# Optimization experiments

Measured on AMD Instinct MI355X. Metric: run time of the kernel, lower is better.

Reference implementation:

```python
import jax, jax.numpy as jnp
import numpy as np

B, N, D = 8, 1024, 512
H, HD = 8, 64          # heads, head_dim
E_EDGES = 4096         # num edges (!= N -> mean-pool branch)
NE, NSH, TOPK = 8, 2, 2  # routed experts, shared experts, top-k
DH = 2 * D             # expert hidden dim
EPS = 1e-5
HALT_BONUS = 0.1
AUX_ALPHA = 0.01


def _ln(x, g, b):
    mu = jnp.mean(x, -1, keepdims=True)
    var = jnp.mean(jnp.square(x - mu), -1, keepdims=True)
    return (x - mu) * jax.lax.rsqrt(var + EPS) * g + b


def setup_inputs() -> dict:
    key = jax.random.key(0)
    ks = jax.random.split(key, 20)
    w = lambda k, shp: jax.random.normal(k, shp, jnp.float32) * 0.02
    return {
        'h': jax.random.normal(ks[0], (B, N, D), jnp.float32),
        'edge_features': jax.random.normal(ks[1], (B, E_EDGES, D), jnp.float32),
        'log_A': jnp.zeros((D,), jnp.float32),
        'B_w': w(ks[2], (D, D)), 'B_b': jnp.zeros((D,), jnp.float32),
        'Wq': w(ks[3], (D, D)), 'bq': jnp.zeros((D,), jnp.float32),
        'Wk': w(ks[4], (D, D)), 'bk': jnp.zeros((D,), jnp.float32),
        'Wv': w(ks[5], (D, D)), 'bv': jnp.zeros((D,), jnp.float32),
        'Wo': w(ks[6], (D, D)), 'bo': jnp.zeros((D,), jnp.float32),
        'n1_g': jnp.ones((D,), jnp.float32), 'n1_b': jnp.zeros((D,), jnp.float32),
        'n2_g': jnp.ones((D,), jnp.float32), 'n2_b': jnp.zeros((D,), jnp.float32),
        'n3_g': jnp.ones((D,), jnp.float32), 'n3_b': jnp.zeros((D,), jnp.float32),
        'gate_w': w(ks[7], (D, NE)), 'gate_b': jnp.zeros((NE,), jnp.float32),
        'eW1': w(ks[8], (NE, D, DH)), 'eb1': jnp.zeros((NE, DH), jnp.float32),
        'eW2': w(ks[9], (NE, DH, D)), 'eb2': jnp.zeros((NE, D), jnp.float32),
        'sW1': w(ks[10], (NSH, D, DH)), 'sb1': jnp.zeros((NSH, DH), jnp.float32),
        'sW2': w(ks[11], (NSH, DH, D)), 'sb2': jnp.zeros((NSH, D), jnp.float32),
        'hW1': w(ks[12], (D, D // 2)), 'hb1': jnp.zeros((D // 2,), jnp.float32),
        'hW2': w(ks[13], (D // 2, 1)), 'hb2': jnp.zeros((1,), jnp.float32),
    }


def reference(h, edge_features, log_A, B_w, B_b, Wq, bq, Wk, bk, Wv, bv, Wo, bo,
              n1_g, n1_b, n2_g, n2_b, n3_g, n3_b, gate_w, gate_b,
              eW1, eb1, eW2, eb2, sW1, sb1, sW2, sb2, hW1, hb1, hW2, hb2):
    # --- LTI: h_decay + mean-pooled edge injection (num_edges != num_nodes) ---
    A = -jnp.exp(log_A)                                   # spectral constraint
    edge_inj = edge_features @ B_w + B_b                  # [B,E,D]
    edge_inj = jnp.mean(edge_inj, axis=1, keepdims=True)  # [B,1,D] broadcast
    h_lti = _ln(A * h + edge_inj, n1_g, n1_b)

    # --- attention (faithful to source: no head/node transpose -> [B,N,H,H] scores) ---
    q = (h_lti @ Wq + bq).reshape(B, N, H, HD)
    k = (h_lti @ Wk + bk).reshape(B, N, H, HD)
    v = (h_lti @ Wv + bv).reshape(B, N, H, HD)
    scores = jnp.einsum('bnhd,bngd->bnhg', q, k) / jnp.sqrt(jnp.float32(HD))
    attn = jax.nn.softmax(scores, axis=-1)                # dropout = identity (eval)
    h_attn = jnp.einsum('bnhg,bngd->bnhd', attn, v).reshape(B, N, D) @ Wo + bo
    h2 = _ln(h_lti + h_attn, n2_g, n2_b)

    # --- SparseMoE: top-k routed + shared experts, load-balance aux loss ---
    x = h2.reshape(-1, D)                                 # [T,D]
    T = x.shape[0]
    probs = jax.nn.softmax(x @ gate_w + gate_b, axis=-1)  # [T,NE]
    topv, topi = jax.lax.top_k(probs, TOPK)
    topv = topv / jnp.sum(topv, -1, keepdims=True)        # renormalize top-k
    w_full = jnp.sum(jax.nn.one_hot(topi, NE, dtype=x.dtype) * topv[..., None], axis=1)  # [T,NE]
    hid = jax.nn.silu(jnp.einsum('td,edh->teh', x, eW1) + eb1)   # [T,NE,DH]
    eout = jnp.einsum('teh,ehd->ted', hid, eW2) + eb2            # [T,NE,D]
    routed = jnp.einsum('te,ted->td', w_full, eout)
    shid = jax.nn.silu(jnp.einsum('td,sdh->tsh', x, sW1) + sb1)
    shared = jnp.sum(jnp.einsum('tsh,shd->tsd', shid, sW2) + sb2, axis=1)
    h_moe = (routed + shared).reshape(B, N, D)
    frac = jnp.mean(jnp.sum(jax.nn.one_hot(topi, NE, dtype=x.dtype), axis=1), axis=0)  # tokens per expert
    pmean = jnp.mean(probs, axis=0)
    moe_loss = AUX_ALPHA * NE * jnp.sum(frac * pmean)

    h3 = _ln(h2 + h_moe, n3_g, n3_b)                      # dropout = identity (eval)

    # --- stability loss (source uses .item() -> detached constant) ---
    stab = jax.lax.stop_gradient(jnp.maximum(jnp.max(jnp.exp(log_A)) - 0.95, 0.0))

    # --- ACT halting (cumsum_halt=None path) ---
    halt_logits = (jnp.tanh(h3 @ hW1 + hb1) @ hW2 + hb2)[..., 0]  # [B,N]
    halt_prob = jax.nn.sigmoid(halt_logits)
    cumsum_halt = halt_prob                                # zeros + prob * active(=1)
    return h3, cumsum_halt, halt_prob, stab + moe_loss
```

## Files before the change

kernel.cpp:

```cpp
#include <hip/hip_runtime.h>
#include <hip/hip_bf16.h>

#define TT 8192
#define DD 512

typedef unsigned short u16;
typedef __attribute__((ext_vector_type(8))) short short8;
typedef __attribute__((ext_vector_type(4))) float f32x4;

__device__ __forceinline__ u16 f2b(float f) {
  union { float f; unsigned int i; } w; w.f = f;
  unsigned int x = w.i;
  unsigned int r = (x + 0x7FFFu + ((x >> 16) & 1u)) >> 16;
  if ((x & 0x7F800000u) == 0x7F800000u) r = x >> 16;
  return (u16)r;
}
__device__ __forceinline__ float b2f(u16 u) {
  union { unsigned int i; float f; } w; w.i = ((unsigned int)u) << 16; return w.f;
}

__device__ __forceinline__ void blockReduce2(float& a, float& b, float* s4a, float* s4b) {
  #pragma unroll
  for (int off = 32; off; off >>= 1) { a += __shfl_xor(a, off); b += __shfl_xor(b, off); }
  int wid = threadIdx.x >> 6;
  if ((threadIdx.x & 63) == 0) { s4a[wid] = a; s4b[wid] = b; }
  __syncthreads();
  a = s4a[0] + s4a[1] + s4a[2] + s4a[3];
  b = s4b[0] + s4b[1] + s4b[2] + s4b[3];
}

__global__ __launch_bounds__(256) void k_zero(float* __restrict__ esum) {
  esum[blockIdx.x * 256 + threadIdx.x] = 0.f;
}

__global__ __launch_bounds__(256) void k_zero4(float4* __restrict__ p) {
  p[(size_t)blockIdx.x * 256 + threadIdx.x] = make_float4(0.f, 0.f, 0.f, 0.f);
}

__global__ __launch_bounds__(256) void k_esum(const float* __restrict__ ef, float* __restrict__ esum) {
  int b = blockIdx.x, ec = blockIdx.y, tid = threadIdx.x;
  float a0 = 0.f, a1 = 0.f;
  const float* base = ef + ((size_t)b * 4096 + (size_t)ec * 128) * 512;
  for (int e = 0; e < 128; ++e) {
    a0 += base[(size_t)e * 512 + tid];
    a1 += base[(size_t)e * 512 + tid + 256];
  }
  atomicAdd(&esum[b * 512 + tid], a0);
  atomicAdd(&esum[b * 512 + tid + 256], a1);
}

__global__ __launch_bounds__(256) void k_einj(const float* __restrict__ esum,
                                              const float* __restrict__ Bw, const float* __restrict__ Bb,
                                              float* __restrict__ einj) {
  int idx = blockIdx.x * 256 + threadIdx.x;
  int b = idx >> 9, dp = idx & 511;
  float a = Bb[dp];
  const float inv = 1.f / 4096.f;
  for (int d = 0; d < 512; ++d)
    a = fmaf(esum[b * 512 + d] * inv, Bw[d * 512 + dp], a);
  einj[idx] = a;
}

__global__ __launch_bounds__(256) void k_wsplit(const float* __restrict__ Wq, const float* __restrict__ Wk,
                                                const float* __restrict__ Wv, const float* __restrict__ Wo,
                                                u16* __restrict__ outh, u16* __restrict__ outl) {
  __shared__ float st[64][65];
  int z = blockIdx.z;
  const float* W = z == 0 ? Wq : (z == 1 ? Wk : (z == 2 ? Wv : Wo));
  int k0 = blockIdx.x << 6, n0 = blockIdx.y << 6;
  int tid = threadIdx.x;
  int r = tid >> 2, c4 = (tid & 3) << 4;
  #pragma unroll
  for (int j = 0; j < 16; j += 4) {
    float4 v = *(const float4*)(W + (size_t)(k0 + r) * 512 + n0 + c4 + j);
    st[c4 + j + 0][r] = v.x; st[c4 + j + 1][r] = v.y;
    st[c4 + j + 2][r] = v.z; st[c4 + j + 3][r] = v.w;
  }
  __syncthreads();
  int n = tid >> 2, kb = (tid & 3) << 4;
  u16 h8[8] __attribute__((aligned(16)));
  u16 l8[8] __attribute__((aligned(16)));
  size_t obase = (size_t)z * 262144 + (size_t)(n0 + n) * 512 + k0 + kb;
  #pragma unroll
  for (int half = 0; half < 2; ++half) {
    #pragma unroll
    for (int j = 0; j < 8; ++j) {
      float val = st[n][kb + half * 8 + j];
      h8[j] = f2b(val);
      l8[j] = f2b(val - b2f(h8[j]));
    }
    *(uint4*)(outh + obase + half * 8) = *(uint4*)h8;
    *(uint4*)(outl + obase + half * 8) = *(uint4*)l8;
  }
}

__global__ __launch_bounds__(256) void k_wt(const float* __restrict__ W, u16* __restrict__ Wt,
                                            int K, int N) {
  __shared__ float st[64][65];
  int z = blockIdx.z;
  W += (size_t)z * K * N; Wt += (size_t)z * K * N;
  int k0 = blockIdx.x << 6, n0 = blockIdx.y << 6;
  int tid = threadIdx.x;
  int r = tid >> 2, c4 = (tid & 3) << 4;
  #pragma unroll
  for (int j = 0; j < 16; j += 4) {
    float4 v = *(const float4*)(W + (size_t)(k0 + r) * N + n0 + c4 + j);
    st[c4 + j + 0][r] = v.x; st[c4 + j + 1][r] = v.y;
    st[c4 + j + 2][r] = v.z; st[c4 + j + 3][r] = v.w;
  }
  __syncthreads();
  int n = tid >> 2, kb = (tid & 3) << 4;
  u16 h8[8] __attribute__((aligned(16)));
  size_t obase = (size_t)(n0 + n) * K + k0 + kb;
  #pragma unroll
  for (int half = 0; half < 2; ++half) {
    #pragma unroll
    for (int j = 0; j < 8; ++j) h8[j] = f2b(st[n][kb + half * 8 + j]);
    *(uint4*)(Wt + obase + half * 8) = *(uint4*)h8;
  }
}

__global__ __launch_bounds__(256) void k_lti(const float* __restrict__ h, const float* __restrict__ lA,
                                             const float* __restrict__ einj,
                                             const float* __restrict__ g, const float* __restrict__ be,
                                             u16* __restrict__ Xh, u16* __restrict__ Xl, int seg0) {
  __shared__ float sa[4], sb[4];
  int rowg = seg0 + blockIdx.x, b = rowg >> 10, tid = threadIdx.x;
  int d0 = tid, d1 = tid + 256;
  size_t gbase = (size_t)rowg * 512;
  size_t lbase = (size_t)blockIdx.x * 512;
  float v0 = -expf(lA[d0]) * h[gbase + d0] + einj[b * 512 + d0];
  float v1 = -expf(lA[d1]) * h[gbase + d1] + einj[b * 512 + d1];
  float s = v0 + v1, ss = v0 * v0 + v1 * v1;
  blockReduce2(s, ss, sa, sb);
  float mu = s * (1.f / 512.f);
  float var = fmaxf(ss * (1.f / 512.f) - mu * mu, 0.f);
  float r = rsqrtf(var + 1e-5f);
  float o0 = (v0 - mu) * r * g[d0] + be[d0];
  float o1 = (v1 - mu) * r * g[d1] + be[d1];
  u16 h0 = f2b(o0), h1 = f2b(o1);
  Xh[lbase + d0] = h0; Xl[lbase + d0] = f2b(o0 - b2f(h0));
  Xh[lbase + d1] = h1; Xl[lbase + d1] = f2b(o1 - b2f(h1));
}

__global__ __launch_bounds__(256) void k_ln_res2(const u16* __restrict__ Xh, const u16* __restrict__ Xl,
                                                 const float* __restrict__ Bv,
                                                 const float* __restrict__ g, const float* __restrict__ be,
                                                 float* __restrict__ outf, u16* __restrict__ outb) {
  __shared__ float sa[4], sb[4];
  int tid = threadIdx.x, d0 = tid, d1 = tid + 256;
  size_t base = (size_t)blockIdx.x * 512;
  float v0 = b2f(Xh[base + d0]) + b2f(Xl[base + d0]) + Bv[base + d0];
  float v1 = b2f(Xh[base + d1]) + b2f(Xl[base + d1]) + Bv[base + d1];
  float s = v0 + v1, ss = v0 * v0 + v1 * v1;
  blockReduce2(s, ss, sa, sb);
  float mu = s * (1.f / 512.f);
  float var = fmaxf(ss * (1.f / 512.f) - mu * mu, 0.f);
  float r = rsqrtf(var + 1e-5f);
  float o0 = (v0 - mu) * r * g[d0] + be[d0];
  float o1 = (v1 - mu) * r * g[d1] + be[d1];
  outf[base + d0] = o0;
  outf[base + d1] = o1;
  if (outb) { outb[base + d0] = f2b(o0); outb[base + d1] = f2b(o1); }
}

__global__ __launch_bounds__(256) void k_ln_res(const float* __restrict__ A, const float* __restrict__ Bv,
                                                const float* __restrict__ g, const float* __restrict__ be,
                                                float* __restrict__ outf) {
  __shared__ float sa[4], sb[4];
  int tid = threadIdx.x, d0 = tid, d1 = tid + 256;
  size_t base = (size_t)blockIdx.x * 512;
  float v0 = A[base + d0] + Bv[base + d0];
  float v1 = A[base + d1] + Bv[base + d1];
  float s = v0 + v1, ss = v0 * v0 + v1 * v1;
  blockReduce2(s, ss, sa, sb);
  float mu = s * (1.f / 512.f);
  float var = fmaxf(ss * (1.f / 512.f) - mu * mu, 0.f);
  float r = rsqrtf(var + 1e-5f);
  outf[base + d0] = (v0 - mu) * r * g[d0] + be[d0];
  outf[base + d1] = (v1 - mu) * r * g[d1] + be[d1];
}

template<int NOUT>
__global__ __launch_bounds__(256) void gemm_sp2(
    const u16* __restrict__ Xh, const u16* __restrict__ Xl, int lda,
    const u16* __restrict__ Wth, const u16* __restrict__ Wtl,
    const float* __restrict__ b0c, const float* __restrict__ b1c, const float* __restrict__ b2c,
    float* __restrict__ C0, float* __restrict__ C1, float* __restrict__ C2) {
  const float* bias = b0c; float* C = C0;
  const u16* Wh = Wth; const u16* Wl = Wtl;
  if (NOUT == 3) {
    int z = blockIdx.z;
    Wh += (size_t)z * 262144; Wl += (size_t)z * 262144;
    if (z == 1) { bias = b1c; C = C1; }
    else if (z == 2) { bias = b2c; C = C2; }
  }
  const int bm = blockIdx.y << 7, bn = blockIdx.x << 7;
  __shared__ u16 Ah[128][40];
  __shared__ u16 Al[128][40];
  __shared__ u16 Bh[128][40];
  __shared__ u16 Bl[128][40];
  const int tid = threadIdx.x;
  const int sr = tid >> 1, sk = (tid & 1) << 4;
  const int wv = tid >> 6, lane = tid & 63, q = lane >> 4, m16 = lane & 15;
  const int wr = (wv >> 1) << 6, wc = (wv & 1) << 6;
  f32x4 acc[4][4];
  #pragma unroll
  for (int m = 0; m < 4; ++m)
    #pragma unroll
    for (int n = 0; n < 4; ++n)
      #pragma unroll
      for (int i = 0; i < 4; ++i) acc[m][n][i] = 0.f;

  for (int k0 = 0; k0 < 512; k0 += 32) {
    __syncthreads();
    const size_t ao_ = (size_t)(bm + sr) * lda + k0 + sk;
    const size_t bo_ = (size_t)(bn + sr) * 512 + k0 + sk;
    *(uint4*)&Ah[sr][sk]     = *(const uint4*)(Xh + ao_);
    *(uint4*)&Ah[sr][sk + 8] = *(const uint4*)(Xh + ao_ + 8);
    *(uint4*)&Al[sr][sk]     = *(const uint4*)(Xl + ao_);
    *(uint4*)&Al[sr][sk + 8] = *(const uint4*)(Xl + ao_ + 8);
    *(uint4*)&Bh[sr][sk]     = *(const uint4*)(Wh + bo_);
    *(uint4*)&Bh[sr][sk + 8] = *(const uint4*)(Wh + bo_ + 8);
    *(uint4*)&Bl[sr][sk]     = *(const uint4*)(Wl + bo_);
    *(uint4*)&Bl[sr][sk + 8] = *(const uint4*)(Wl + bo_ + 8);
    __syncthreads();
    short8 ah[4], al[4];
    #pragma unroll
    for (int m = 0; m < 4; ++m) {
      ah[m] = *(const short8*)&Ah[wr + m * 16 + m16][q * 8];
      al[m] = *(const short8*)&Al[wr + m * 16 + m16][q * 8];
    }
    #pragma unroll
    for (int n = 0; n < 4; ++n) {
      short8 bh = *(const short8*)&Bh[wc + n * 16 + m16][q * 8];
      short8 bl = *(const short8*)&Bl[wc + n * 16 + m16][q * 8];
      #pragma unroll
      for (int m = 0; m < 4; ++m) {
        acc[m][n] = __builtin_amdgcn_mfma_f32_16x16x32_bf16(ah[m], bh, acc[m][n], 0, 0, 0);
        acc[m][n] = __builtin_amdgcn_mfma_f32_16x16x32_bf16(al[m], bh, acc[m][n], 0, 0, 0);
        acc[m][n] = __builtin_amdgcn_mfma_f32_16x16x32_bf16(ah[m], bl, acc[m][n], 0, 0, 0);
      }
    }
  }
  #pragma unroll
  for (int n = 0; n < 4; ++n) {
    int col = bn + wc + n * 16 + m16;
    float bb = bias[col];
    #pragma unroll
    for (int m = 0; m < 4; ++m) {
      #pragma unroll
      for (int i = 0; i < 4; ++i) {
        int rl = bm + wr + m * 16 + q * 4 + i;
        C[(size_t)rl * 512 + col] = acc[m][n][i] + bb;
      }
    }
  }
}

__global__ __launch_bounds__(64) void k_attn(const float* __restrict__ q, const float* __restrict__ k,
                                             const float* __restrict__ v,
                                             u16* __restrict__ aohl) {
  __shared__ float qs[512], ks[512], vs[512], at[64];
  size_t t = blockIdx.x;
  int lane = threadIdx.x;
  for (int i = lane; i < 512; i += 64) {
    qs[i] = q[t * 512 + i]; ks[i] = k[t * 512 + i]; vs[i] = v[t * 512 + i];
  }
  __syncthreads();
  int h = lane >> 3, g = lane & 7;
  float s = 0.f;
  #pragma unroll 8
  for (int d = 0; d < 64; ++d) s = fmaf(qs[h * 64 + d], ks[g * 64 + d], s);
  s *= 0.125f;
  float m = s;
  #pragma unroll
  for (int off = 1; off < 8; off <<= 1) m = fmaxf(m, __shfl_xor(m, off));
  float ex = expf(s - m);
  float sum = ex;
  #pragma unroll
  for (int off = 1; off < 8; off <<= 1) sum += __shfl_xor(sum, off);
  at[lane] = ex / sum;
  __syncthreads();
  #pragma unroll
  for (int j = 0; j < 8; ++j) {
    int d = lane + j * 64, hh = d >> 6, hd = d & 63;
    float acc = 0.f;
    #pragma unroll
    for (int gg = 0; gg < 8; ++gg) acc = fmaf(at[hh * 8 + gg], vs[gg * 64 + hd], acc);
    u16 hi = f2b(acc);
    aohl[t * 1024 + d] = hi;
    aohl[t * 1024 + 512 + d] = f2b(acc - b2f(hi));
  }
}

__global__ __launch_bounds__(256) void k_gateA(const float* __restrict__ h2, const float* __restrict__ gw,
                                               const float* __restrict__ gb, float* __restrict__ probs,
                                               int* __restrict__ sel, float2* __restrict__ wpair) {
  int lane = threadIdx.x & 63, wid = threadIdx.x >> 6;
  int t = blockIdx.x * 4 + wid;
  const float* x = h2 + (size_t)t * 512;
  float acc[8] = {};
  for (int d = lane; d < 512; d += 64) {
    float xv = x[d];
    float4 g0 = *(const float4*)(gw + d * 8);
    float4 g1 = *(const float4*)(gw + d * 8 + 4);
    acc[0] = fmaf(xv, g0.x, acc[0]); acc[1] = fmaf(xv, g0.y, acc[1]);
    acc[2] = fmaf(xv, g0.z, acc[2]); acc[3] = fmaf(xv, g0.w, acc[3]);
    acc[4] = fmaf(xv, g1.x, acc[4]); acc[5] = fmaf(xv, g1.y, acc[5]);
    acc[6] = fmaf(xv, g1.z, acc[6]); acc[7] = fmaf(xv, g1.w, acc[7]);
  }
  #pragma unroll
  for (int off = 32; off; off >>= 1)
    #pragma unroll
    for (int e = 0; e < 8; ++e) acc[e] += __shfl_xor(acc[e], off);
  if (lane == 0) {
    float m = -1e30f;
    #pragma unroll
    for (int e = 0; e < 8; ++e) { acc[e] += gb[e]; m = fmaxf(m, acc[e]); }
    float p[8], sum = 0.f;
    #pragma unroll
    for (int e = 0; e < 8; ++e) { p[e] = expf(acc[e] - m); sum += p[e]; }
    float inv = 1.f / sum;
    #pragma unroll
    for (int e = 0; e < 8; ++e) { p[e] *= inv; probs[t * 8 + e] = p[e]; }
    int i1 = 0; float m1 = p[0];
    #pragma unroll
    for (int e = 1; e < 8; ++e) if (p[e] > m1) { m1 = p[e]; i1 = e; }
    int i2 = -1; float m2 = -1.f;
    #pragma unroll
    for (int e = 0; e < 8; ++e) if (e != i1 && p[e] > m2) { m2 = p[e]; i2 = e; }
    if (i2 < 0) i2 = (i1 + 1) & 7;
    float den = m1 + m2;
    float invs = (den > 0.f) ? 1.f / den : 0.f;
    sel[t] = i1 | (i2 << 4);
    wpair[t] = make_float2(m1 * invs, m2 * invs);
  }
}

__global__ __launch_bounds__(256) void k_gateB(const int* __restrict__ sel, const float2* __restrict__ wpair,
                                               int* __restrict__ toklist, float* __restrict__ wlist,
                                               int* __restrict__ cnt) {
  int e = blockIdx.x;
  int tid = threadIdx.x, lane = tid & 63, wv = tid >> 6;
  __shared__ int wsum[4];
  int base = 0;
  for (int t0 = 0; t0 < 8192; t0 += 256) {
    int t = t0 + tid;
    int s = sel[t];
    int i1 = s & 15, i2 = (s >> 4) & 15;
    bool f = (i1 == e) || (i2 == e);
    float wt = (i1 == e) ? wpair[t].x : ((i2 == e) ? wpair[t].y : 0.f);
    unsigned long long m = __ballot(f);
    int rank = __popcll(m & ((1ull << lane) - 1ull));
    int wtot = __popcll(m);
    if (lane == 0) wsum[wv] = wtot;
    __syncthreads();
    int prev = 0;
    for (int ww = 0; ww < wv; ++ww) prev += wsum[ww];
    int tot = wsum[0] + wsum[1] + wsum[2] + wsum[3];
    if (f) {
      int pos = base + prev + rank;
      toklist[e * 8192 + pos] = t;
      wlist[e * 8192 + pos] = wt;
    }
    base += tot;
    __syncthreads();
  }
  if (tid == 0) cnt[e] = base;
}

template<int XMODE, int ACT, int OUTMODE, int EXPERT>
__global__ __launch_bounds__(256) void mfma_gemm(
    const float* __restrict__ Xf, const u16* __restrict__ Xb,
    const float* __restrict__ Wg, const float* __restrict__ biasg,
    float* __restrict__ C, u16* __restrict__ C16,
    const int* __restrict__ toklist, const float* __restrict__ wlist,
    const int* __restrict__ cnt, int M, int K, int N, int chunk0,
    size_t hidstride, float* __restrict__ moe) {
  int e = EXPERT ? blockIdx.z : 0;
  const float* W = Wg + (size_t)e * K * N;
  const float* bias = biasg + (size_t)e * N;
  int Mloc = M;
  if (EXPERT) {
    int ce = cnt[e]; if (ce > 8192) ce = 8192;
    Mloc = ce - chunk0;
    if (XMODE == 1) Xb += (size_t)e * hidstride;
    if (OUTMODE == 2) C16 += (size_t)e * hidstride;
  }
  const int bm = blockIdx.y << 6, bn = blockIdx.x << 6;
  if (EXPERT && bm >= Mloc) return;
  __shared__ u16 As[64][40];
  __shared__ u16 Bs[64][40];
  __shared__ int rows[64];
  const int tid = threadIdx.x;
  if (EXPERT && XMODE == 2 && tid < 64) {
    int ce = cnt[e]; if (ce > 8192) ce = 8192;
    int r = chunk0 + bm + tid;
    rows[tid] = toklist[e * 8192 + (r < ce ? r : chunk0)] & 8191;
  }
  const int srow = tid >> 2;
  const int skg = (tid & 3) << 3;
  const int wv = tid >> 6, lane = tid & 63, q = lane >> 4, m16 = lane & 15;
  f32x4 acc[4];
  #pragma unroll
  for (int c = 0; c < 4; ++c)
    #pragma unroll
    for (int i = 0; i < 4; ++i) acc[c][i] = 0.f;

  for (int k0 = 0; k0 < K; k0 += 32) {
    __syncthreads();
    {
      u16 a8[8] __attribute__((aligned(16)));
      if (XMODE == 1) {
        *(uint4*)a8 = *(const uint4*)(Xb + (size_t)(bm + srow) * K + k0 + skg);
      } else {
        const float* src = (XMODE == 2) ? (Xf + (size_t)rows[srow] * K + k0 + skg)
                                        : (Xf + (size_t)(bm + srow) * K + k0 + skg);
        float4 x0 = *(const float4*)(src);
        float4 x1 = *(const float4*)(src + 4);
        a8[0] = f2b(x0.x); a8[1] = f2b(x0.y); a8[2] = f2b(x0.z); a8[3] = f2b(x0.w);
        a8[4] = f2b(x1.x); a8[5] = f2b(x1.y); a8[6] = f2b(x1.z); a8[7] = f2b(x1.w);
      }
      *(uint4*)&As[srow][skg] = *(uint4*)a8;
    }
    {
      u16 b8[8] __attribute__((aligned(16)));
      const float* src = W + (size_t)(k0 + skg) * N + bn + srow;
      #pragma unroll
      for (int j = 0; j < 8; ++j) b8[j] = f2b(src[(size_t)j * N]);
      *(uint4*)&Bs[srow][skg] = *(uint4*)b8;
    }
    __syncthreads();
    short8 af = *(const short8*)&As[wv * 16 + m16][q * 8];
    #pragma unroll
    for (int c = 0; c < 4; ++c) {
      short8 bf = *(const short8*)&Bs[c * 16 + m16][q * 8];
      acc[c] = __builtin_amdgcn_mfma_f32_16x16x32_bf16(af, bf, acc[c], 0, 0, 0);
    }
  }
  #pragma unroll
  for (int c = 0; c < 4; ++c) {
    int col = bn + c * 16 + m16;
    float bb = bias[col];
    #pragma unroll
    for (int i = 0; i < 4; ++i) {
      int rl = bm + wv * 16 + q * 4 + i;
      if (EXPERT && rl >= Mloc) continue;
      float v = acc[c][i] + bb;
      if (ACT == 1) v = v / (1.f + expf(-v));
      else if (ACT == 2) v = tanhf(v);
      if (OUTMODE == 0) C[(size_t)rl * N + col] = v;
      else if (OUTMODE == 1) C[(size_t)rl * N + col] += v;
      else if (OUTMODE == 2) C16[(size_t)rl * N + col] = f2b(v);
      else {
        int rg = chunk0 + rl;
        int tok = toklist[e * 8192 + rg] & 8191;
        float wt = wlist[e * 8192 + rg];
        atomicAdd(&moe[(size_t)tok * 512 + col], v * wt);
      }
    }
  }
}

template<int XMODE, int ACT, int OUTMODE, int EXPERT>
__global__ __launch_bounds__(512, 4) void mfma_gemm3(
    const u16* __restrict__ Xb, const u16* __restrict__ Wt, const float* __restrict__ biasg,
    float* __restrict__ C, u16* __restrict__ C16,
    const int* __restrict__ toklist, const float* __restrict__ wlist,
    const int* __restrict__ cnt, int M, int K, int N, int chunk0,
    size_t hidstride, float* __restrict__ moe) {
  int e = EXPERT ? blockIdx.z : 0;
  const u16* W = Wt + (size_t)e * K * N;
  const float* bias = biasg + (size_t)e * N;
  int Mloc = M;
  if (EXPERT == 1) {
    int ce = cnt[e]; if (ce > 8192) ce = 8192;
    Mloc = ce - chunk0;
  }
  if (EXPERT) {
    if (XMODE == 3) Xb += (size_t)e * hidstride;
    if (OUTMODE == 2) C16 += (size_t)e * hidstride;
  }
  const int bm = blockIdx.y << 7, bn = blockIdx.x << 7;
  if (EXPERT == 1 && bm >= Mloc) return;
  __shared__ u16 As[2][128][40];
  __shared__ u16 Bs[2][128][40];
  __shared__ int rows[128];
  const int tid = threadIdx.x;
  if (EXPERT == 1 && XMODE == 2) {
    if (tid < 128) {
      int ce = cnt[e]; if (ce > 8192) ce = 8192;
      int r = chunk0 + bm + tid;
      rows[tid] = toklist[e * 8192 + (r < ce ? r : chunk0)] & 8191;
    }
    __syncthreads();
  }
  const int sr = tid >> 2, sk = (tid & 3) << 3;
  const int wv = tid >> 6, lane = tid & 63, q = lane >> 4, m16 = lane & 15;
  const int wr = (wv >> 2) << 6;
  const int wc = (wv & 3) << 5;
  const u16* arow = (XMODE == 2) ? (Xb + (size_t)rows[sr] * K) : (Xb + (size_t)(bm + sr) * K);
  const u16* brow = W + (size_t)(bn + sr) * K;
  f32x4 acc[4][2];
  #pragma unroll
  for (int m = 0; m < 4; ++m)
    #pragma unroll
    for (int n = 0; n < 2; ++n)
      #pragma unroll
      for (int i = 0; i < 4; ++i) acc[m][n][i] = 0.f;

  uint4 ar = *(const uint4*)(arow + sk);
  uint4 br = *(const uint4*)(brow + sk);
  *(uint4*)&As[0][sr][sk] = ar;
  *(uint4*)&Bs[0][sr][sk] = br;
  __syncthreads();
  int cur = 0;
  for (int k0 = 0; k0 < K; k0 += 32) {
    if (k0 + 32 < K) {
      ar = *(const uint4*)(arow + k0 + 32 + sk);
      br = *(const uint4*)(brow + k0 + 32 + sk);
    }
    short8 af[4];
    #pragma unroll
    for (int m = 0; m < 4; ++m)
      af[m] = *(const short8*)&As[cur][wr + m * 16 + m16][q * 8];
    short8 bf[2];
    #pragma unroll
    for (int n = 0; n < 2; ++n)
      bf[n] = *(const short8*)&Bs[cur][wc + n * 16 + m16][q * 8];
    #pragma unroll
    for (int n = 0; n < 2; ++n)
      #pragma unroll
      for (int m = 0; m < 4; ++m)
        acc[m][n] = __builtin_amdgcn_mfma_f32_16x16x32_bf16(af[m], bf[n], acc[m][n], 0, 0, 0);
    if (k0 + 32 < K) {
      *(uint4*)&As[cur ^ 1][sr][sk] = ar;
      *(uint4*)&Bs[cur ^ 1][sr][sk] = br;
      __syncthreads();
      cur ^= 1;
    }
  }
  #pragma unroll
  for (int n = 0; n < 2; ++n) {
    int col = bn + wc + n * 16 + m16;
    float bb = bias[col];
    #pragma unroll
    for (int m = 0; m < 4; ++m) {
      #pragma unroll
      for (int i = 0; i < 4; ++i) {
        int rl = bm + wr + m * 16 + q * 4 + i;
        if (EXPERT == 1 && rl >= Mloc) continue;
        float v = acc[m][n][i] + bb;
        if (ACT == 1) v = v / (1.f + expf(-v));
        if (OUTMODE == 0) C[(size_t)rl * N + col] = v;
        else if (OUTMODE == 1) C[(size_t)rl * N + col] += v;
        else if (OUTMODE == 2) C16[(size_t)rl * N + col] = f2b(v);
        else if (OUTMODE == 3) {
          int rg = chunk0 + rl;
          int tok = toklist[e * 8192 + rg] & 8191;
          float wt = wlist[e * 8192 + rg];
          atomicAdd(&moe[(size_t)tok * 512 + col], v * wt);
        } else {
          atomicAdd(&C[(size_t)rl * N + col], v);
        }
      }
    }
  }
}

__global__ __launch_bounds__(256) void k_halt(const u16* __restrict__ hh, const float* __restrict__ hW2,
                                              const float* __restrict__ hb2, float* __restrict__ out) {
  int lane = threadIdx.x & 63, wid = threadIdx.x >> 6;
  int t = blockIdx.x * 4 + wid;
  const u16* x = hh + (size_t)t * 256;
  float a = b2f(x[lane]) * hW2[lane] + b2f(x[lane + 64]) * hW2[lane + 64] +
            b2f(x[lane + 128]) * hW2[lane + 128] + b2f(x[lane + 192]) * hW2[lane + 192];
  #pragma unroll
  for (int off = 32; off; off >>= 1) a += __shfl_xor(a, off);
  if (lane == 0) {
    float p = 1.f / (1.f + expf(-(a + hb2[0])));
    out[4194304 + t] = p;
    out[4194304 + 8192 + t] = p;
  }
}

__global__ __launch_bounds__(256) void k_final(const float* __restrict__ probs, const int* __restrict__ cnt,
                                               const float* __restrict__ lA, float* __restrict__ out) {
  __shared__ float sp[4][8];
  __shared__ float sm[4];
  int tid = threadIdx.x, lane = tid & 63, wid = tid >> 6;
  float part[8] = {};
  for (int i = tid; i < 8192; i += 256) {
    const float* p = probs + i * 8;
    #pragma unroll
    for (int e = 0; e < 8; ++e) part[e] += p[e];
  }
  #pragma unroll
  for (int off = 32; off; off >>= 1)
    #pragma unroll
    for (int e = 0; e < 8; ++e) part[e] += __shfl_xor(part[e], off);
  float mx = 0.f;
  for (int d = tid; d < 512; d += 256) mx = fmaxf(mx, expf(lA[d]));
  #pragma unroll
  for (int off = 32; off; off >>= 1) mx = fmaxf(mx, __shfl_xor(mx, off));
  if (lane == 0) {
    #pragma unroll
    for (int e = 0; e < 8; ++e) sp[wid][e] = part[e];
    sm[wid] = mx;
  }
  __syncthreads();
  if (tid == 0) {
    float loss = 0.f;
    for (int e = 0; e < 8; ++e) {
      float pm = (sp[0][e] + sp[1][e] + sp[2][e] + sp[3][e]) * (1.f / 8192.f);
      int c = cnt[e]; if (c > 8192) c = 8192;
      loss += (float)c * (1.f / 8192.f) * pm;
    }
    loss *= 0.01f * 8.f;
    float mall = fmaxf(fmaxf(sm[0], sm[1]), fmaxf(sm[2], sm[3]));
    out[4194304 + 16384] = fmaxf(mall - 0.95f, 0.f) + loss;
  }
}

extern "C" void kernel_launch(void* const* d_in, const int* in_sizes, int n_in,
                              void* d_out, int out_size, void* d_ws, size_t ws_size,
                              hipStream_t stream) {
  const float* h   = (const float*)d_in[0];
  const float* ef  = (const float*)d_in[1];
  const float* lA  = (const float*)d_in[2];
  const float* Bw  = (const float*)d_in[3];
  const float* Bb  = (const float*)d_in[4];
  const float* Wq  = (const float*)d_in[5];  const float* bq  = (const float*)d_in[6];
  const float* Wk  = (const float*)d_in[7];  const float* bk  = (const float*)d_in[8];
  const float* Wv  = (const float*)d_in[9];  const float* bv  = (const float*)d_in[10];
  const float* Wo  = (const float*)d_in[11]; const float* bo  = (const float*)d_in[12];
  const float* n1g = (const float*)d_in[13]; const float* n1b = (const float*)d_in[14];
  const float* n2g = (const float*)d_in[15]; const float* n2b = (const float*)d_in[16];
  const float* n3g = (const float*)d_in[17]; const float* n3b = (const float*)d_in[18];
  const float* gw  = (const float*)d_in[19]; const float* gb  = (const float*)d_in[20];
  const float* eW1 = (const float*)d_in[21]; const float* eb1 = (const float*)d_in[22];
  const float* eW2 = (const float*)d_in[23]; const float* eb2 = (const float*)d_in[24];
  const float* sW1 = (const float*)d_in[25]; const float* sb1 = (const float*)d_in[26];
  const float* sW2 = (const float*)d_in[27]; const float* sb2 = (const float*)d_in[28];
  const float* hW1 = (const float*)d_in[29]; const float* hb1 = (const float*)d_in[30];
  const float* hW2 = (const float*)d_in[31]; const float* hb2 = (const float*)d_in[32];
  float* out = (float*)d_out;
  float* ws = (float*)d_ws;

  const size_t R = (size_t)TT * DD;
  const size_t SM = 155648 + 73744;
  size_t wsf = ws_size / 4;
  int S; size_t ARENA;
  bool FAST;
  if (wsf >= 6 * R + SM)      { S = 8192; ARENA = 4 * R; FAST = true; }
  else if (wsf >= 3 * R + SM) { S = 2048; ARENA = R; FAST = false; }
  else                        { S = 512;  ARENA = 1048576; FAST = false; }
  const int CAPE = (int)(ARENA / 4096);
  const int NCH  = 8192 / CAPE;
  const size_t HIDSTRIDE = (size_t)CAPE * 1024;
  const int CAPS = (ARENA / 512 >= 8192) ? 8192 : (int)(ARENA / 512);

  float* f_h2  = ws;
  float* f_moe = ws + R;
  float* arena = ws + 2 * R;
  const size_t SD = (size_t)S * 512;
  u16* f_xh = (u16*)arena;
  u16* f_xl = f_xh + SD;
  float* f_q = arena + SD;
  float* f_k = arena + 2 * SD;
  float* f_v = arena + 3 * SD;
  u16* f_aohl = (u16*)f_q;
  float* f_hp = f_k;
  u16* f_wh = (u16*)f_moe;
  u16* f_wl = f_wh + 4 * 262144;
  u16* f_hid = (u16*)arena;
  u16* f_hh  = (u16*)arena;
  u16* a16 = (u16*)arena;
  const int CAPE_F = 2048, NCH_F = 4;
  const size_t HSF = (size_t)CAPE_F * 1024;
  u16* f_hidF = a16;
  u16* f_eW1t = a16 + 16777216;
  u16* f_eW2t = a16 + 20971520;
  u16* f_h2b  = a16 + 25165824;
  u16* f_sW1t = a16 + 29360128;
  u16* f_sW2t = a16 + 30408704;
  float* smr = ws + 2 * R + ARENA;
  float* f_esum = smr;
  float* f_einj = smr + 4096;
  float* f_probs = smr + 8192;
  float2* f_wpair = (float2*)(smr + 8192 + 65536);
  float* f_wlist = smr + 8192 + 65536 + 16384;
  int* ip = (int*)(smr + 8192 + 65536 + 16384 + 65536);
  int* sel = ip; int* cnt = ip + 8192; int* toklist = ip + 8192 + 16;

  k_zero<<<16, 256, 0, stream>>>(f_esum);
  k_esum<<<dim3(8, 32), 256, 0, stream>>>(ef, f_esum);
  k_einj<<<16, 256, 0, stream>>>(f_esum, Bw, Bb, f_einj);
  k_wsplit<<<dim3(8, 8, 4), 256, 0, stream>>>(Wq, Wk, Wv, Wo, f_wh, f_wl);

  for (int s = 0; s < TT / S; ++s) {
    int seg0 = s * S;
    k_lti<<<S, 256, 0, stream>>>(h, lA, f_einj, n1g, n1b, f_xh, f_xl, seg0);
    gemm_sp2<3><<<dim3(4, S / 128, 3), 256, 0, stream>>>(
        f_xh, f_xl, 512, f_wh, f_wl, bq, bk, bv, f_q, f_k, f_v);
    k_attn<<<S, 64, 0, stream>>>(f_q, f_k, f_v, f_aohl);
    gemm_sp2<1><<<dim3(4, S / 128, 1), 256, 0, stream>>>(
        f_aohl, f_aohl + 512, 1024, f_wh + 3 * 262144, f_wl + 3 * 262144,
        bo, nullptr, nullptr, f_hp, nullptr, nullptr);
    k_ln_res2<<<S, 256, 0, stream>>>(f_xh, f_xl, f_hp, n2g, n2b,
                                     f_h2 + (size_t)seg0 * 512,
                                     FAST ? f_h2b + (size_t)seg0 * 512 : nullptr);
  }

  k_gateA<<<TT / 4, 256, 0, stream>>>(f_h2, gw, gb, f_probs, sel, f_wpair);
  k_gateB<<<8, 256, 0, stream>>>(sel, f_wpair, toklist, f_wlist, cnt);

  if (FAST) {
    k_zero4<<<4096, 256, 0, stream>>>((float4*)f_moe);
    k_wt<<<dim3(8, 16, 8), 256, 0, stream>>>(eW1, f_eW1t, 512, 1024);
    k_wt<<<dim3(16, 8, 8), 256, 0, stream>>>(eW2, f_eW2t, 1024, 512);
    k_wt<<<dim3(8, 16, 2), 256, 0, stream>>>(sW1, f_sW1t, 512, 1024);
    k_wt<<<dim3(16, 8, 2), 256, 0, stream>>>(sW2, f_sW2t, 1024, 512);

    mfma_gemm3<1,1,2,2><<<dim3(8, 64, 2), 512, 0, stream>>>(
        f_h2b, f_sW1t, sb1, nullptr, f_hidF, nullptr, nullptr, nullptr,
        TT, 512, 1024, 0, (size_t)TT * 1024, nullptr);
    mfma_gemm3<3,0,4,2><<<dim3(4, 64, 2), 512, 0, stream>>>(
        f_hidF, f_sW2t, sb2, f_moe, nullptr, nullptr, nullptr, nullptr,
        TT, 1024, 512, 0, (size_t)TT * 1024, nullptr);

    for (int c = 0; c < NCH_F; ++c) {
      mfma_gemm3<2,1,2,1><<<dim3(8, CAPE_F / 128, 8), 512, 0, stream>>>(
          f_h2b, f_eW1t, eb1, nullptr, f_hidF, toklist, nullptr, cnt,
          CAPE_F, 512, 1024, c * CAPE_F, HSF, nullptr);
      mfma_gemm3<3,0,3,1><<<dim3(4, CAPE_F / 128, 8), 512, 0, stream>>>(
          f_hidF, f_eW2t, eb2, nullptr, nullptr, toklist, f_wlist, cnt,
          CAPE_F, 1024, 512, c * CAPE_F, HSF, f_moe);
    }
  } else {
    for (int sx = 0; sx < 2; ++sx)
      for (int c = 0; c < TT / CAPS; ++c) {
        const float* xs = f_h2 + (size_t)c * CAPS * 512;
        float* ms = f_moe + (size_t)c * CAPS * 512;
        mfma_gemm<0,1,2,0><<<dim3(16, CAPS / 64), 256, 0, stream>>>(
            xs, nullptr, sW1 + (size_t)sx * 524288, sb1 + sx * 1024,
            nullptr, f_hid, nullptr, nullptr, nullptr, CAPS, 512, 1024, 0, 0, nullptr);
        if (sx == 0)
          mfma_gemm<1,0,0,0><<<dim3(8, CAPS / 64), 256, 0, stream>>>(
              nullptr, f_hid, sW2, sb2, ms, nullptr, nullptr, nullptr, nullptr, CAPS, 1024, 512, 0, 0, nullptr);
        else
          mfma_gemm<1,0,1,0><<<dim3(8, CAPS / 64), 256, 0, stream>>>(
              nullptr, f_hid, sW2 + 524288, sb2 + 512, ms, nullptr, nullptr, nullptr, nullptr, CAPS, 1024, 512, 0, 0, nullptr);
      }
    for (int c = 0; c < NCH; ++c) {
      mfma_gemm<2,1,2,1><<<dim3(16, CAPE / 64, 8), 256, 0, stream>>>(
          f_h2, nullptr, eW1, eb1, nullptr, f_hid, toklist, nullptr, cnt,
          CAPE, 512, 1024, c * CAPE, HIDSTRIDE, nullptr);
      mfma_gemm<1,0,3,1><<<dim3(8, CAPE / 64, 8), 256, 0, stream>>>(
          nullptr, f_hid, eW2, eb2, nullptr, nullptr, toklist, f_wlist, cnt,
          CAPE, 1024, 512, c * CAPE, HIDSTRIDE, f_moe);
    }
  }

  k_ln_res<<<TT, 256, 0, stream>>>(f_h2, f_moe, n3g, n3b, out);
  mfma_gemm<0,2,2,0><<<dim3(4, 128), 256, 0, stream>>>(
      out, nullptr, hW1, hb1, nullptr, f_hh, nullptr, nullptr, nullptr, TT, 512, 256, 0, 0, nullptr);
  k_halt<<<TT / 4, 256, 0, stream>>>(f_hh, hW2, hb2, out);
  k_final<<<1, 256, 0, stream>>>(f_probs, cnt, lA, out);
}
```

Before: 713.7 us.

## Double-buffer split-bf16 attention GEMM and move halting head to bf16 MFMA path

The split-precision attention projection GEMM now uses 512 threads with a 4x2 wave layout and double-buffered shared memory, prefetching the next K-slice into registers while the MFMAs run. This is meant to hide global-load latency and drop one barrier per iteration. In the fast path, the final layernorm also writes a bf16 copy of its output. The halting MLP's first layer then runs through the bf16 mfma_gemm3 kernel with a transposed weight and a new tanh activation in the epilogue. That trades some precision in the halting head and adds a small transpose launch.

```diff
diff --git a/kernel.cpp b/kernel.cpp
--- a/kernel.cpp
+++ b/kernel.cpp
@@ -166,7 +166,7 @@
 
 __global__ __launch_bounds__(256) void k_ln_res(const float* __restrict__ A, const float* __restrict__ Bv,
                                                 const float* __restrict__ g, const float* __restrict__ be,
-                                                float* __restrict__ outf) {
+                                                float* __restrict__ outf, u16* __restrict__ outb) {
   __shared__ float sa[4], sb[4];
   int tid = threadIdx.x, d0 = tid, d1 = tid + 256;
   size_t base = (size_t)blockIdx.x * 512;
@@ -177,12 +177,15 @@
   float mu = s * (1.f / 512.f);
   float var = fmaxf(ss * (1.f / 512.f) - mu * mu, 0.f);
   float r = rsqrtf(var + 1e-5f);
-  outf[base + d0] = (v0 - mu) * r * g[d0] + be[d0];
-  outf[base + d1] = (v1 - mu) * r * g[d1] + be[d1];
+  float o0 = (v0 - mu) * r * g[d0] + be[d0];
+  float o1 = (v1 - mu) * r * g[d1] + be[d1];
+  outf[base + d0] = o0;
+  outf[base + d1] = o1;
+  if (outb) { outb[base + d0] = f2b(o0); outb[base + d1] = f2b(o1); }
 }
 
 template<int NOUT>
-__global__ __launch_bounds__(256) void gemm_sp2(
+__global__ __launch_bounds__(512, 4) void gemm_sp3(
     const u16* __restrict__ Xh, const u16* __restrict__ Xl, int lda,
     const u16* __restrict__ Wth, const u16* __restrict__ Wtl,
     const float* __restrict__ b0c, const float* __restrict__ b1c, const float* __restrict__ b2c,
@@ -196,55 +199,72 @@
     else if (z == 2) { bias = b2c; C = C2; }
   }
   const int bm = blockIdx.y << 7, bn = blockIdx.x << 7;
-  __shared__ u16 Ah[128][40];
-  __shared__ u16 Al[128][40];
-  __shared__ u16 Bh[128][40];
-  __shared__ u16 Bl[128][40];
+  __shared__ u16 Ah[2][128][40];
+  __shared__ u16 Al[2][128][40];
+  __shared__ u16 Bh[2][128][40];
+  __shared__ u16 Bl[2][128][40];
   const int tid = threadIdx.x;
-  const int sr = tid >> 1, sk = (tid & 1) << 4;
+  const int sr = tid >> 2, sk = (tid & 3) << 3;
   const int wv = tid >> 6, lane = tid & 63, q = lane >> 4, m16 = lane & 15;
-  const int wr = (wv >> 1) << 6, wc = (wv & 1) << 6;
-  f32x4 acc[4][4];
+  const int wr = (wv >> 2) << 6;
+  const int wc = (wv & 3) << 5;
+  const u16* ahr = Xh + (size_t)(bm + sr) * lda;
+  const u16* alr = Xl + (size_t)(bm + sr) * lda;
+  const u16* bhr = Wh + (size_t)(bn + sr) * 512;
+  const u16* blr = Wl + (size_t)(bn + sr) * 512;
+  f32x4 acc[4][2];
   #pragma unroll
   for (int m = 0; m < 4; ++m)
     #pragma unroll
-    for (int n = 0; n < 4; ++n)
+    for (int n = 0; n < 2; ++n)
       #pragma unroll
       for (int i = 0; i < 4; ++i) acc[m][n][i] = 0.f;
 
+  uint4 rah = *(const uint4*)(ahr + sk);
+  uint4 ral = *(const uint4*)(alr + sk);
+  uint4 rbh = *(const uint4*)(bhr + sk);
+  uint4 rbl = *(const uint4*)(blr + sk);
+  *(uint4*)&Ah[0][sr][sk] = rah;
+  *(uint4*)&Al[0][sr][sk] = ral;
+  *(uint4*)&Bh[0][sr][sk] = rbh;
+  *(uint4*)&Bl[0][sr][sk] = rbl;
+  __syncthreads();
+  int cur = 0;
   for (int k0 = 0; k0 < 512; k0 += 32) {
-    __syncthreads();
-    const size_t ao_ = (size_t)(bm + sr) * lda + k0 + sk;
-    const size_t bo_ = (size_t)(bn + sr) * 512 + k0 + sk;
-    *(uint4*)&Ah[sr][sk]     = *(const uint4*)(Xh + ao_);
-    *(uint4*)&Ah[sr][sk + 8] = *(const uint4*)(Xh + ao_ + 8);
-    *(uint4*)&Al[sr][sk]     = *(const uint4*)(Xl + ao_);
-    *(uint4*)&Al[sr][sk + 8] = *(const uint4*)(Xl + ao_ + 8);
-    *(uint4*)&Bh[sr][sk]     = *(const uint4*)(Wh + bo_);
-    *(uint4*)&Bh[sr][sk + 8] = *(const uint4*)(Wh + bo_ + 8);
-    *(uint4*)&Bl[sr][sk]     = *(const uint4*)(Wl + bo_);
-    *(uint4*)&Bl[sr][sk + 8] = *(const uint4*)(Wl + bo_ + 8);
-    __syncthreads();
-    short8 ah[4], al[4];
+    if (k0 + 32 < 512) {
+      rah = *(const uint4*)(ahr + k0 + 32 + sk);
+      ral = *(const uint4*)(alr + k0 + 32 + sk);
+      rbh = *(const uint4*)(bhr + k0 + 32 + sk);
+      rbl = *(const uint4*)(blr + k0 + 32 + sk);
+    }
+    short8 ahf[4], alf[4];
     #pragma unroll
     for (int m = 0; m < 4; ++m) {
-      ah[m] = *(const short8*)&Ah[wr + m * 16 + m16][q * 8];
-      al[m] = *(const short8*)&Al[wr + m * 16 + m16][q * 8];
-    }
-    #pragma unroll
-    for (int n = 0; n < 4; ++n) {
-      short8 bh = *(const short8*)&Bh[wc + n * 16 + m16][q * 8];
-      short8 bl = *(const short8*)&Bl[wc + n * 16 + m16][q * 8];
+      ahf[m] = *(const short8*)&Ah[cur][wr + m * 16 + m16][q * 8];
+      alf[m] = *(const short8*)&Al[cur][wr + m * 16 + m16][q * 8];
+    }
+    #pragma unroll
+    for (int n = 0; n < 2; ++n) {
+      short8 bhf = *(const short8*)&Bh[cur][wc + n * 16 + m16][q * 8];
+      short8 blf = *(const short8*)&Bl[cur][wc + n * 16 + m16][q * 8];
       #pragma unroll
       for (int m = 0; m < 4; ++m) {
-        acc[m][n] = __builtin_amdgcn_mfma_f32_16x16x32_bf16(ah[m], bh, acc[m][n], 0, 0, 0);
-        acc[m][n] = __builtin_amdgcn_mfma_f32_16x16x32_bf16(al[m], bh, acc[m][n], 0, 0, 0);
-        acc[m][n] = __builtin_amdgcn_mfma_f32_16x16x32_bf16(ah[m], bl, acc[m][n], 0, 0, 0);
+        acc[m][n] = __builtin_amdgcn_mfma_f32_16x16x32_bf16(ahf[m], bhf, acc[m][n], 0, 0, 0);
+        acc[m][n] = __builtin_amdgcn_mfma_f32_16x16x32_bf16(alf[m], bhf, acc[m][n], 0, 0, 0);
+        acc[m][n] = __builtin_amdgcn_mfma_f32_16x16x32_bf16(ahf[m], blf, acc[m][n], 0, 0, 0);
       }
     }
-  }
-  #pragma unroll
-  for (int n = 0; n < 4; ++n) {
+    if (k0 + 32 < 512) {
+      *(uint4*)&Ah[cur ^ 1][sr][sk] = rah;
+      *(uint4*)&Al[cur ^ 1][sr][sk] = ral;
+      *(uint4*)&Bh[cur ^ 1][sr][sk] = rbh;
+      *(uint4*)&Bl[cur ^ 1][sr][sk] = rbl;
+      __syncthreads();
+      cur ^= 1;
+    }
+  }
+  #pragma unroll
+  for (int n = 0; n < 2; ++n) {
     int col = bn + wc + n * 16 + m16;
     float bb = bias[col];
     #pragma unroll
@@ -553,6 +573,7 @@
         if (EXPERT == 1 && rl >= Mloc) continue;
         float v = acc[m][n][i] + bb;
         if (ACT == 1) v = v / (1.f + expf(-v));
+        else if (ACT == 2) v = tanhf(v);
         if (OUTMODE == 0) C[(size_t)rl * N + col] = v;
         else if (OUTMODE == 1) C[(size_t)rl * N + col] += v;
         else if (OUTMODE == 2) C16[(size_t)rl * N + col] = f2b(v);
@@ -685,6 +706,9 @@
   u16* f_h2b  = a16 + 25165824;
   u16* f_sW1t = a16 + 29360128;
   u16* f_sW2t = a16 + 30408704;
+  u16* f_h3b  = a16;
+  u16* f_hW1t = a16 + 4194304;
+  u16* f_hh3  = a16 + 4325376;
   float* smr = ws + 2 * R + ARENA;
   float* f_esum = smr;
   float* f_einj = smr + 4096;
@@ -702,10 +726,10 @@
   for (int s = 0; s < TT / S; ++s) {
     int seg0 = s * S;
     k_lti<<<S, 256, 0, stream>>>(h, lA, f_einj, n1g, n1b, f_xh, f_xl, seg0);
-    gemm_sp2<3><<<dim3(4, S / 128, 3), 256, 0, stream>>>(
+    gemm_sp3<3><<<dim3(4, S / 128, 3), 512, 0, stream>>>(
         f_xh, f_xl, 512, f_wh, f_wl, bq, bk, bv, f_q, f_k, f_v);
     k_attn<<<S, 64, 0, stream>>>(f_q, f_k, f_v, f_aohl);
-    gemm_sp2<1><<<dim3(4, S / 128, 1), 256, 0, stream>>>(
+    gemm_sp3<1><<<dim3(4, S / 128, 1), 512, 0, stream>>>(
         f_aohl, f_aohl + 512, 1024, f_wh + 3 * 262144, f_wl + 3 * 262144,
         bo, nullptr, nullptr, f_hp, nullptr, nullptr);
     k_ln_res2<<<S, 256, 0, stream>>>(f_xh, f_xl, f_hp, n2g, n2b,
@@ -738,6 +762,13 @@
           f_hidF, f_eW2t, eb2, nullptr, nullptr, toklist, f_wlist, cnt,
           CAPE_F, 1024, 512, c * CAPE_F, HSF, f_moe);
     }
+
+    k_ln_res<<<TT, 256, 0, stream>>>(f_h2, f_moe, n3g, n3b, out, f_h3b);
+    k_wt<<<dim3(8, 4, 1), 256, 0, stream>>>(hW1, f_hW1t, 512, 256);
+    mfma_gemm3<1,2,2,0><<<dim3(2, 64), 512, 0, stream>>>(
+        f_h3b, f_hW1t, hb1, nullptr, f_hh3, nullptr, nullptr, nullptr,
+        TT, 512, 256, 0, 0, nullptr);
+    k_halt<<<TT / 4, 256, 0, stream>>>(f_hh3, hW2, hb2, out);
   } else {
     for (int sx = 0; sx < 2; ++sx)
       for (int c = 0; c < TT / CAPS; ++c) {
@@ -761,11 +792,11 @@
           nullptr, f_hid, eW2, eb2, nullptr, nullptr, toklist, f_wlist, cnt,
           CAPE, 1024, 512, c * CAPE, HIDSTRIDE, f_moe);
     }
-  }
-
-  k_ln_res<<<TT, 256, 0, stream>>>(f_h2, f_moe, n3g, n3b, out);
-  mfma_gemm<0,2,2,0><<<dim3(4, 128), 256, 0, stream>>>(
-      out, nullptr, hW1, hb1, nullptr, f_hh, nullptr, nullptr, nullptr, TT, 512, 256, 0, 0, nullptr);
-  k_halt<<<TT / 4, 256, 0, stream>>>(f_hh, hW2, hb2, out);
+    k_ln_res<<<TT, 256, 0, stream>>>(f_h2, f_moe, n3g, n3b, out, nullptr);
+    mfma_gemm<0,2,2,0><<<dim3(4, 128), 256, 0, stream>>>(
+        out, nullptr, hW1, hb1, nullptr, f_hh, nullptr, nullptr, nullptr, TT, 512, 256, 0, 0, nullptr);
+    k_halt<<<TT / 4, 256, 0, stream>>>(f_hh, hW2, hb2, out);
+  }
+
   k_final<<<1, 256, 0, stream>>>(f_probs, cnt, lA, out);
 }
```

After: 691.1 us. 3.2% less time.
